# Optimization experiments

Measured on AMD Instinct MI355X. Metric: run time of the kernel, lower is better.

## Reference

```python
import jax, jax.numpy as jnp
import numpy as np


def setup_inputs() -> dict:
    key = jax.random.key(0)
    k1, k2, k3, k4 = jax.random.split(key, 4)
    B, S, D = 8, 2048, 512
    scale = 1.0 / np.sqrt(D)
    return {
        "x": jax.random.normal(k1, (B, S, D), dtype=jnp.float32),
        "WQ": jax.random.normal(k2, (D, D), dtype=jnp.float32) * scale,
        "WK": jax.random.normal(k3, (D, D), dtype=jnp.float32) * scale,
        "WV": jax.random.normal(k4, (D, D), dtype=jnp.float32) * scale,
    }


def reference(x, WQ, WK, WV):
    # x: [B, S, D]; single-head scaled dot-product self-attention
    Q = jnp.einsum("bsd,de->bse", x, WQ)
    K = jnp.einsum("bsd,de->bse", x, WK)
    V = jnp.einsum("bsd,de->bse", x, WV)
    d_k = jnp.asarray(K.shape[-1], dtype=x.dtype)
    scores = jnp.einsum("bqd,bkd->bqk", Q, K) / jnp.sqrt(d_k)  # [B,S,S]
    weights = jax.nn.softmax(scores, axis=-1)
    return jnp.einsum("bqk,bkd->bqd", weights, V)
```

## Files before the change

### kernel.cpp

```cpp
#include <hip/hip_runtime.h>
#include <cstdint>
#include <cstddef>

#define B_ 8
#define S_ 2048
#define D_ 512

typedef float f32x4 __attribute__((ext_vector_type(4)));
typedef __bf16 bf16x8 __attribute__((ext_vector_type(8)));

__device__ __forceinline__ unsigned short f2bf(float f) {
    unsigned u = __builtin_bit_cast(unsigned, f);
    u += 0x7FFFu + ((u >> 16) & 1u);
    return (unsigned short)(u >> 16);
}

__device__ __forceinline__ void gld_lds16(const void* g, void* l) {
    __builtin_amdgcn_global_load_lds(
        (__attribute__((address_space(1))) void*)g,
        (__attribute__((address_space(3))) void*)l,
        16, 0, 0);
}

__global__ __launch_bounds__(256) void gemm_bt(
    const unsigned short* __restrict__ A,
    const unsigned short* __restrict__ B,
    void* __restrict__ Cv,
    unsigned short* __restrict__ Cv2,
    float* __restrict__ rs_part,
    int K, int lda, int ldb, int ldc,
    long long sA, long long sB, long long sC,
    float scale, int mode, int ntn, int nbatch)
{
    __shared__ __align__(16) unsigned short lA[128 * 32];
    __shared__ __align__(16) unsigned short lB[128 * 32];

    const int lin = blockIdx.x;
    const int bz  = lin % nbatch;
    const int t   = lin / nbatch;
    const int tn  = t % ntn;
    const int tm  = t / ntn;

    A += (long long)bz * sA;
    B += (long long)bz * sB;
    const int m0 = tm * 128;
    const int n0 = tn * 128;
    const int tid  = threadIdx.x;
    const int lane = tid & 63;
    const int wave = tid >> 6;
    const int wm = (wave & 1) * 64;
    const int wn = (wave >> 1) * 64;

    f32x4 acc[4][4] = {};

    const int bo0 = wave * 2048;
    const int bo1 = bo0 + 1024;
    const int o0 = bo0 + lane * 16;
    const int o1 = bo1 + lane * 16;
    const int r0 = o0 >> 6, cp0 = (o0 & 63) >> 4;
    const int r1 = o1 >> 6, cp1 = (o1 & 63) >> 4;
    const int c0 = (cp0 ^ ((r0 >> 1) & 3)) << 3;
    const int c1 = (cp1 ^ ((r1 >> 1) & 3)) << 3;

    const unsigned short* A0 = A + (size_t)(m0 + r0) * lda + c0;
    const unsigned short* A1 = A + (size_t)(m0 + r1) * lda + c1;
    const unsigned short* B0 = B + (size_t)(n0 + r0) * ldb + c0;
    const unsigned short* B1 = B + (size_t)(n0 + r1) * ldb + c1;

    char* lAc = (char*)lA;
    char* lBc = (char*)lB;

    const int fr  = lane & 15;
    const int g   = lane >> 4;
    const int sx  = (g ^ ((fr >> 1) & 3)) << 3;

    for (int k0 = 0; k0 < K; k0 += 32) {
        __syncthreads();
        gld_lds16(A0 + k0, lAc + bo0);
        gld_lds16(A1 + k0, lAc + bo1);
        gld_lds16(B0 + k0, lBc + bo0);
        gld_lds16(B1 + k0, lBc + bo1);
        __syncthreads();

        bf16x8 af[4], bfv[4];
        #pragma unroll
        for (int tt = 0; tt < 4; ++tt) {
            af[tt]  = *(const bf16x8*)&lA[(wm + tt * 16 + fr) * 32 + sx];
            bfv[tt] = *(const bf16x8*)&lB[(wn + tt * 16 + fr) * 32 + sx];
        }
        #pragma unroll
        for (int mt = 0; mt < 4; ++mt)
            #pragma unroll
            for (int nt = 0; nt < 4; ++nt)
                acc[mt][nt] = __builtin_amdgcn_mfma_f32_16x16x32_bf16(
                    af[mt], bfv[nt], acc[mt][nt], 0, 0, 0);
    }

    const int rb = g << 2;

    if (mode == 1) {
        #pragma unroll
        for (int mt = 0; mt < 4; ++mt)
            #pragma unroll
            for (int nt = 0; nt < 4; ++nt)
                #pragma unroll
                for (int r = 0; r < 4; ++r)
                    acc[mt][nt][r] = __expf(acc[mt][nt][r] * scale);

        unsigned short* C = (unsigned short*)Cv + (long long)bz * sC;
        #pragma unroll
        for (int mt = 0; mt < 4; ++mt)
            #pragma unroll
            for (int nt = 0; nt < 4; ++nt) {
                const int gc = n0 + wn + nt * 16 + fr;
                #pragma unroll
                for (int r = 0; r < 4; ++r)
                    C[(size_t)(m0 + wm + mt * 16 + rb + r) * ldc + gc] =
                        f2bf(acc[mt][nt][r]);
            }

        float* rp = rs_part + (((long long)bz * S_) << 5) + tn * 2 + (wn >> 6);
        #pragma unroll
        for (int mt = 0; mt < 4; ++mt)
            #pragma unroll
            for (int r = 0; r < 4; ++r) {
                float s = acc[mt][0][r] + acc[mt][1][r] +
                          acc[mt][2][r] + acc[mt][3][r];
                s += __shfl_xor(s, 8);
                s += __shfl_xor(s, 4);
                s += __shfl_xor(s, 2);
                s += __shfl_xor(s, 1);
                if (fr == 0)
                    rp[(long long)(m0 + wm + mt * 16 + rb + r) << 5] = s;
            }
    } else if (mode == 3) {
        if (tn >= 8) {
            #pragma unroll
            for (int mt = 0; mt < 4; ++mt) {
                const int s0q = m0 + wm + mt * 16 + rb;
                const int b   = s0q >> 11;
                const int se  = s0q & (S_ - 1);
                #pragma unroll
                for (int nt = 0; nt < 4; ++nt) {
                    const int d = (n0 - 1024) + wn + nt * 16 + fr;
                    ushort4 u;
                    u.x = f2bf(acc[mt][nt][0]);
                    u.y = f2bf(acc[mt][nt][1]);
                    u.z = f2bf(acc[mt][nt][2]);
                    u.w = f2bf(acc[mt][nt][3]);
                    *(ushort4*)&Cv2[((size_t)b * D_ + d) * S_ + se] = u;
                }
            }
        } else {
            unsigned short* C = (unsigned short*)Cv;
            #pragma unroll
            for (int mt = 0; mt < 4; ++mt)
                #pragma unroll
                for (int nt = 0; nt < 4; ++nt) {
                    const int gc = n0 + wn + nt * 16 + fr;
                    #pragma unroll
                    for (int r = 0; r < 4; ++r)
                        C[(size_t)(m0 + wm + mt * 16 + rb + r) * ldc + gc] =
                            f2bf(acc[mt][nt][r]);
                }
        }
    } else {
        float* C = (float*)Cv + (long long)bz * sC;
        #pragma unroll
        for (int nt = 0; nt < 4; ++nt) {
            const int q = n0 + wn + nt * 16 + fr;
            const float* rp = rs_part + (((long long)bz * S_ + q) << 5);
            float ssum = 0.f;
            #pragma unroll
            for (int pq = 0; pq < 8; ++pq) {
                const float4 p4 = *(const float4*)(rp + 4 * pq);
                ssum += (p4.x + p4.y) + (p4.z + p4.w);
            }
            const float inv = __builtin_amdgcn_rcpf(ssum);
            #pragma unroll
            for (int mt = 0; mt < 4; ++mt) {
                const int d0 = m0 + wm + mt * 16 + rb;
                float4 o;
                o.x = acc[mt][nt][0] * inv;
                o.y = acc[mt][nt][1] * inv;
                o.z = acc[mt][nt][2] * inv;
                o.w = acc[mt][nt][3] * inv;
                *(float4*)&C[(size_t)q * ldc + d0] = o;
            }
        }
    }
}

__global__ __launch_bounds__(256) void convert_x4(const float* __restrict__ x,
                                                  unsigned short* __restrict__ xb) {
    const size_t i = ((size_t)blockIdx.x * 256 + threadIdx.x) * 4;
    const float4 f = *(const float4*)(x + i);
    ushort4 u;
    u.x = f2bf(f.x); u.y = f2bf(f.y); u.z = f2bf(f.z); u.w = f2bf(f.w);
    *(ushort4*)(xb + i) = u;
}

__global__ __launch_bounds__(256) void convert_w(const float* __restrict__ WQ,
                                                 const float* __restrict__ WK,
                                                 const float* __restrict__ WV,
                                                 unsigned short* __restrict__ WT) {
    const int o = blockIdx.x * 256 + threadIdx.x;
    const float* W = blockIdx.y == 0 ? WQ : (blockIdx.y == 1 ? WK : WV);
    const int e = o >> 9, d = o & (D_ - 1);
    WT[(size_t)blockIdx.y * D_ * D_ + o] = f2bf(W[d * D_ + e]);
}

extern "C" void kernel_launch(void* const* d_in, const int* in_sizes, int n_in,
                              void* d_out, int out_size, void* d_ws, size_t ws_size,
                              hipStream_t stream)
{
    const float* x  = (const float*)d_in[0];
    const float* WQ = (const float*)d_in[1];
    const float* WK = (const float*)d_in[2];
    const float* WV = (const float*)d_in[3];

    unsigned short* ws  = (unsigned short*)d_ws;
    const size_t NX = (size_t)B_ * S_ * D_;
    unsigned short* xb  = ws;
    unsigned short* wtb = xb + NX;
    unsigned short* qk  = wtb + 3 * D_ * D_;
    unsigned short* vtb = qk + NX * 2;
    unsigned short* sb  = vtb + NX;
    float* rsp = (float*)(sb + (size_t)B_ * S_ * S_);

    convert_x4<<<dim3((unsigned)(NX / 4 / 256)), 256, 0, stream>>>(x, xb);
    convert_w<<<dim3(D_ * D_ / 256, 3), 256, 0, stream>>>(WQ, WK, WV, wtb);

    gemm_bt<<<dim3((B_ * S_ / 128) * (3 * D_ / 128)), 256, 0, stream>>>(
        xb, wtb, qk, vtb, nullptr, D_, D_, D_, 2 * D_,
        0, 0, 0, 1.0f, 3,  3 * D_ / 128,  1);

    gemm_bt<<<dim3(B_ * (S_ / 128) * (S_ / 128)), 256, 0, stream>>>(
        qk , qk + D_ , sb, nullptr, rsp, D_, 2 * D_, 2 * D_, S_,
        (long long)S_ * 2 * D_, (long long)S_ * 2 * D_, (long long)S_ * S_,
        0.04419417382415922f, 1,  S_ / 128,  B_);

    gemm_bt<<<dim3(B_ * (D_ / 128) * (S_ / 128)), 256, 0, stream>>>(
        vtb, sb, d_out, nullptr, rsp, S_, S_, S_, D_,
        (long long)D_ * S_, (long long)S_ * S_, (long long)S_ * D_,
        1.0f, 0,  S_ / 128,  B_);
}
```

Measured before the change: 255.6 us.

## Load MFMA operands directly from global memory, dropping LDS staging

The GEMM stops staging A and B tiles through shared memory with global_load_lds and barriers. Each wave now loads its bf16x8 MFMA fragments straight from global memory, relying on caches for reuse across waves. The k-loop is unrolled by 4 and launch bounds ask for 3 blocks per CU. This removes the two barriers per k-step and the LDS traffic, but each tile element is now fetched by two waves instead of once per block, and the per-lane reads are strided 16-byte loads that may coalesce poorly.

```diff
diff --git a/kernel.cpp b/kernel.cpp
--- a/kernel.cpp
+++ b/kernel.cpp
@@ -15,14 +15,7 @@
     return (unsigned short)(u >> 16);
 }
 
-__device__ __forceinline__ void gld_lds16(const void* g, void* l) {
-    __builtin_amdgcn_global_load_lds(
-        (__attribute__((address_space(1))) void*)g,
-        (__attribute__((address_space(3))) void*)l,
-        16, 0, 0);
-}
-
-__global__ __launch_bounds__(256) void gemm_bt(
+__global__ __launch_bounds__(256, 3) void gemm_bt(
     const unsigned short* __restrict__ A,
     const unsigned short* __restrict__ B,
     void* __restrict__ Cv,
@@ -32,9 +25,6 @@
     long long sA, long long sB, long long sC,
     float scale, int mode, int ntn, int nbatch)
 {
-    __shared__ __align__(16) unsigned short lA[128 * 32];
-    __shared__ __align__(16) unsigned short lB[128 * 32];
-
     const int lin = blockIdx.x;
     const int bz  = lin % nbatch;
     const int t   = lin / nbatch;
@@ -51,43 +41,23 @@
     const int wm = (wave & 1) * 64;
     const int wn = (wave >> 1) * 64;
 
+    const int fr = lane & 15;
+    const int g  = lane >> 4;
+
     f32x4 acc[4][4] = {};
 
-    const int bo0 = wave * 2048;
-    const int bo1 = bo0 + 1024;
-    const int o0 = bo0 + lane * 16;
-    const int o1 = bo1 + lane * 16;
-    const int r0 = o0 >> 6, cp0 = (o0 & 63) >> 4;
-    const int r1 = o1 >> 6, cp1 = (o1 & 63) >> 4;
-    const int c0 = (cp0 ^ ((r0 >> 1) & 3)) << 3;
-    const int c1 = (cp1 ^ ((r1 >> 1) & 3)) << 3;
-
-    const unsigned short* A0 = A + (size_t)(m0 + r0) * lda + c0;
-    const unsigned short* A1 = A + (size_t)(m0 + r1) * lda + c1;
-    const unsigned short* B0 = B + (size_t)(n0 + r0) * ldb + c0;
-    const unsigned short* B1 = B + (size_t)(n0 + r1) * ldb + c1;
-
-    char* lAc = (char*)lA;
-    char* lBc = (char*)lB;
-
-    const int fr  = lane & 15;
-    const int g   = lane >> 4;
-    const int sx  = (g ^ ((fr >> 1) & 3)) << 3;
-
+    const unsigned short* Ap = A + (size_t)(m0 + wm + fr) * lda + (g << 3);
+    const unsigned short* Bp = B + (size_t)(n0 + wn + fr) * ldb + (g << 3);
+
+    #pragma unroll 4
     for (int k0 = 0; k0 < K; k0 += 32) {
-        __syncthreads();
-        gld_lds16(A0 + k0, lAc + bo0);
-        gld_lds16(A1 + k0, lAc + bo1);
-        gld_lds16(B0 + k0, lBc + bo0);
-        gld_lds16(B1 + k0, lBc + bo1);
-        __syncthreads();
-
         bf16x8 af[4], bfv[4];
         #pragma unroll
-        for (int tt = 0; tt < 4; ++tt) {
-            af[tt]  = *(const bf16x8*)&lA[(wm + tt * 16 + fr) * 32 + sx];
-            bfv[tt] = *(const bf16x8*)&lB[(wn + tt * 16 + fr) * 32 + sx];
-        }
+        for (int mt = 0; mt < 4; ++mt)
+            af[mt] = *(const bf16x8*)(Ap + (size_t)mt * 16 * lda + k0);
+        #pragma unroll
+        for (int nt = 0; nt < 4; ++nt)
+            bfv[nt] = *(const bf16x8*)(Bp + (size_t)nt * 16 * ldb + k0);
         #pragma unroll
         for (int mt = 0; mt < 4; ++mt)
             #pragma unroll
```

Result: slower. 457.6 us (+79.0%).
